# Performance work log

Hardware: AMD Instinct MI355X
Metric: run time of the kernel (lower is better)

Reference implementation:

```python
import jax, jax.numpy as jnp
import numpy as np

B, T, C, E = 2, 100, 80, 32
MH = MW = 64
IN_H = IN_W = 640.0
IOU_FACTOR, CLS_FACTOR, TOPK = 6.0, 0.5, 10
EPS = 1e-9


def get_anchors_and_scalers(fmaps, in_h, in_w):
    anchors, scalers = [], []
    for fh, fw in fmaps:
        stride = in_h / fh
        ys = (np.arange(fh) + 0.5) * stride
        xs = (np.arange(fw) + 0.5) * stride
        gy, gx = np.meshgrid(ys, xs, indexing='ij')
        anchors.append(np.stack([gx, gy], -1).reshape(-1, 2))
        scalers.append(np.full(fh * fw, stride))
    return (np.concatenate(anchors).astype(np.float32),
            np.concatenate(scalers).astype(np.float32))


def setup_inputs() -> dict:
    key = jax.random.key(0)
    ks = jax.random.split(key, 8)
    anchors_np, scalers_np = get_anchors_and_scalers([(80, 80), (40, 40), (20, 20)], IN_H, IN_W)
    anchors = jnp.asarray(anchors_np)
    scalers = jnp.asarray(scalers_np)
    A = anchors.shape[0]
    cls_logits = jax.random.normal(ks[0], (B, A, C), jnp.float32)
    wh = jax.random.uniform(ks[1], (B, A, 2), jnp.float32, 16.0, 160.0)
    ctr = anchors[None] + jax.random.normal(ks[2], (B, A, 2), jnp.float32) * 8.0
    pred_boxes = jnp.clip(jnp.concatenate([ctr - wh / 2, ctr + wh / 2], -1), 0.0, IN_W)
    mask_embs = jax.random.normal(ks[3], (B, A, E), jnp.float32)
    protos = jax.random.normal(ks[4], (B, MH, MW, E), jnp.float32)
    tl = jax.random.uniform(ks[5], (B, T, 2), jnp.float32, 0.0, 560.0)
    twh = jax.random.uniform(ks[6], (B, T, 2), jnp.float32, 30.0, 240.0)
    target_bbox = jnp.concatenate([tl, jnp.minimum(tl + twh, IN_W)], -1)
    target_cls = jax.random.randint(ks[7], (B, T), 0, C, jnp.int32)
    target_masks = (jax.random.uniform(jax.random.fold_in(key, 7), (B, MH, MW, T)) > 0.5).astype(jnp.float32)
    return {'cls_logits': cls_logits, 'pred_boxes': pred_boxes, 'mask_embs': mask_embs,
            'protos': protos, 'target_cls': target_cls, 'target_bbox': target_bbox,
            'target_masks': target_masks, 'anchors': anchors, 'scalers': scalers}


def _ciou_pairwise(gt, pr):
    # gt [B,T,4], pr [B,A,4] -> [B,T,A]
    g = gt[:, :, None, :]
    p = pr[:, None, :, :]
    ix1 = jnp.maximum(g[..., 0], p[..., 0]); iy1 = jnp.maximum(g[..., 1], p[..., 1])
    ix2 = jnp.minimum(g[..., 2], p[..., 2]); iy2 = jnp.minimum(g[..., 3], p[..., 3])
    inter = jnp.clip(ix2 - ix1, 0.0) * jnp.clip(iy2 - iy1, 0.0)
    wg = g[..., 2] - g[..., 0]; hg = g[..., 3] - g[..., 1]
    wp = p[..., 2] - p[..., 0]; hp = p[..., 3] - p[..., 1]
    union = wg * hg + wp * hp - inter + EPS
    iou = inter / union
    cw = jnp.maximum(g[..., 2], p[..., 2]) - jnp.minimum(g[..., 0], p[..., 0])
    ch = jnp.maximum(g[..., 3], p[..., 3]) - jnp.minimum(g[..., 1], p[..., 1])
    c2 = cw * cw + ch * ch + EPS
    rho2 = ((g[..., 0] + g[..., 2] - p[..., 0] - p[..., 2]) ** 2 +
            (g[..., 1] + g[..., 3] - p[..., 1] - p[..., 3]) ** 2) / 4.0
    v = (4.0 / (jnp.pi ** 2)) * (jnp.arctan(wg / (hg + EPS)) - jnp.arctan(wp / (hp + EPS))) ** 2
    alpha = jax.lax.stop_gradient(v / (1.0 - iou + v + EPS))
    return iou - rho2 / c2 - alpha * v


def _bbox_mask(boxes, mh, mw, in_h, in_w):
    # boxes [B,A,4] pixel xyxy -> [B,A,mh,mw] binary inside-box mask on mask grid
    sx, sy = mw / in_w, mh / in_h
    x1, y1, x2, y2 = boxes[..., 0] * sx, boxes[..., 1] * sy, boxes[..., 2] * sx, boxes[..., 3] * sy
    rows = jnp.arange(mh, dtype=boxes.dtype)
    cols = jnp.arange(mw, dtype=boxes.dtype)
    rm = (rows >= y1[..., None]) & (rows < y2[..., None])  # [B,A,mh]
    cm = (cols >= x1[..., None]) & (cols < x2[..., None])  # [B,A,mw]
    return (rm[..., :, None] & cm[..., None, :]).astype(boxes.dtype)


def _assign_and_build(cls_logits, pred_boxes, mask_embs, protos,
                      target_cls, target_bbox, target_masks, anchors, scalers):
    Bn, A, Cn = cls_logits.shape
    mh, mw = protos.shape[1], protos.shape[2]
    # --- task-aligned assigner ---
    lt, rb = target_bbox[:, :, None, :2], target_bbox[:, :, None, 2:]
    deltas = jnp.concatenate([anchors[None, None] - lt, rb - anchors[None, None]], -1)
    grid_mask = (jnp.min(deltas, -1) > 0).astype(cls_logits.dtype)  # [B,T,A]
    iou_mat = jnp.clip(_ciou_pairwise(target_bbox, pred_boxes), 0.0, 1.0)  # [B,T,A]
    cls_prob = jax.nn.sigmoid(cls_logits)  # [B,A,C]
    oh_t = jax.nn.one_hot(target_cls, Cn, dtype=cls_prob.dtype)  # [B,T,C]
    cls_mat = jnp.einsum('btc,bac->bta', oh_t, cls_prob)  # [B,T,A]
    tmat = grid_mask * (iou_mat ** IOU_FACTOR) * (cls_mat ** CLS_FACTOR)
    kth = jax.lax.top_k(tmat, TOPK)[0][..., -1:]  # [B,T,1]
    topk_targets = jnp.where((tmat >= kth) & (tmat > 0), tmat, 0.0)
    unique_idx = jnp.argmax(topk_targets, axis=1)  # [B,A] best GT per anchor
    valid = (jnp.sum(topk_targets, axis=1) > 0).astype(cls_logits.dtype)  # [B,A]
    align_bbox = jnp.take_along_axis(target_bbox, jnp.broadcast_to(unique_idx[..., None], (Bn, A, 4)), axis=1)
    align_cls_idx = jnp.take_along_axis(target_cls, unique_idx, axis=1)  # [B,A]
    max_target = jnp.max(tmat, axis=-1, keepdims=True)
    max_iou = jnp.max(iou_mat, axis=-1, keepdims=True)
    norm_term = tmat / (max_target + EPS) * max_iou  # [B,T,A]
    norm_g = jnp.take_along_axis(jnp.transpose(norm_term, (0, 2, 1)), unique_idx[..., None], axis=2)  # [B,A,1]
    align_cls = jax.nn.one_hot(align_cls_idx, Cn, dtype=cls_logits.dtype) * norm_g * valid[..., None]
    # --- loss-target assembly (compute_loss body) ---
    align_bbox_scaled = align_bbox / scalers[None, :, None]
    boxes_scaled = pred_boxes / scalers[None, :, None]
    box_target = jnp.concatenate([align_bbox_scaled, valid[..., None], align_cls], -1)
    box_mask = _bbox_mask(align_bbox, mh, mw, IN_H, IN_W)  # [B,A,mh,mw]
    valid_seg = box_mask * valid[..., None, None]
    seg_pred = jax.nn.sigmoid(jnp.einsum('bne,bhwe->bnhw', mask_embs, protos)) * valid_seg
    seg_pred = seg_pred.reshape(Bn, A, mh * mw)
    masks_t = jnp.transpose(target_masks, (0, 3, 1, 2))  # [B,T,mh,mw]
    idx4 = jnp.broadcast_to(unique_idx[..., None, None], (Bn, A, mh, mw))
    align_seg = (jnp.take_along_axis(masks_t, idx4, axis=1) * valid_seg).reshape(Bn, A, mh * mw)
    area = ((align_bbox[..., 2] - align_bbox[..., 0]) * (align_bbox[..., 3] - align_bbox[..., 1])
            / (IN_W * IN_H))
    seg_target = jnp.concatenate([area[..., None], valid[..., None], align_seg], -1)
    return jnp.concatenate([boxes_scaled, cls_logits, box_target, seg_pred, seg_target], -1)


def reference(cls_logits, pred_boxes, mask_embs, protos, target_cls, target_bbox,
              target_masks, anchors, scalers):
    return _assign_and_build(cls_logits, pred_boxes, mask_embs, protos,
                             target_cls, target_bbox, target_masks, anchors, scalers)
```

## Files before the change

kernel.cpp:

```cpp
#include <hip/hip_runtime.h>
#include <math.h>

#define A_TOT 8400
#define B_N   2
#define T_N   100
#define C_N   80
#define E_N   32
#define MH_N  64
#define MW_N  64
#define ROW_N 8363
#define NROWS (B_N*A_TOT)
#define EPSF  1e-9f
#define PARAM_STRIDE 12
#define COMP_CAP 1536
#define NEGINF -1e30f

__global__ __launch_bounds__(256) void k_prep(
    const float* __restrict__ pred_boxes, const float* __restrict__ target_bbox,
    float* __restrict__ pred_atan, float* __restrict__ tgt_atan) {
  int i = blockIdx.x * 256 + threadIdx.x;
  if (i < NROWS) {
    float4 pb = *(const float4*)(pred_boxes + (size_t)i*4);
    pred_atan[i] = atanf((pb.z - pb.x) / ((pb.w - pb.y) + EPSF));
  }
  if (i < B_N*T_N) {
    float4 g = *(const float4*)(target_bbox + i*4);
    tgt_atan[i] = atanf((g.z - g.x) / ((g.w - g.y) + EPSF));
  }
}

__device__ __forceinline__ float2 tmat_eval(
    float gx1, float gy1, float gx2, float gy2,
    float ax,  float ay,
    float px1, float py1, float px2, float py2,
    float cl, float atg, float atp) {
  float ix1 = fmaxf(gx1,px1), iy1 = fmaxf(gy1,py1);
  float ix2 = fminf(gx2,px2), iy2 = fminf(gy2,py2);
  float inter = fmaxf(ix2-ix1,0.f) * fmaxf(iy2-iy1,0.f);
  float wg = gx2-gx1, hg = gy2-gy1, wp = px2-px1, hp = py2-py1;
  float uni = wg*hg + wp*hp - inter + EPSF;
  float iou = inter / uni;
  float cw = fmaxf(gx2,px2) - fminf(gx1,px1);
  float ch = fmaxf(gy2,py2) - fminf(gy1,py1);
  float c2 = cw*cw + ch*ch + EPSF;
  float dx = gx1+gx2-px1-px2, dy = gy1+gy2-py1-py2;
  float rho2 = (dx*dx + dy*dy) * 0.25f;
  float da = atg - atp;
  float v  = 0.4052847345693511f * da * da;
  float alpha = v / (1.f - iou + v + EPSF);
  float ciou = iou - rho2/c2 - alpha*v;
  float iouc = fminf(fmaxf(ciou, 0.f), 1.f);

  float tm = 0.f;
  if (ax > gx1 && ay > gy1 && ax < gx2 && ay < gy2) {
    float cp = 1.f / (1.f + expf(-cl));
    float i2 = iouc * iouc;
    tm = i2*i2*i2 * sqrtf(cp);
  }
  return make_float2(tm, iouc);
}

__global__ __launch_bounds__(512) void k_score(
    const float* __restrict__ cls_logits, const float* __restrict__ pred_boxes,
    const float* __restrict__ target_bbox, const int* __restrict__ target_cls,
    const float* __restrict__ anchors,
    const float* __restrict__ pred_atan, const float* __restrict__ tgt_atan,
    float* __restrict__ tmat,
    float* __restrict__ kth, float* __restrict__ maxt, float* __restrict__ maxiou) {
  int bt   = blockIdx.x;
  int b    = bt / T_N;
  int tid  = threadIdx.x;
  int lane = tid & 63, wid = tid >> 6;
  __shared__ float comp[COMP_CAP];
  __shared__ float redm[8], redi[8];
  __shared__ float wtop[8][10];
  __shared__ int   cnt;
  if (tid == 0) cnt = 0;
  __syncthreads();

  float4 g  = *(const float4*)(target_bbox + bt*4);
  int    tc = target_cls[bt];
  float atg = tgt_atan[bt];
  float* trow = tmat + (size_t)bt * A_TOT;

  float lm = 0.f, li = 0.f;
  for (int a = tid; a < A_TOT; a += 512) {
    float ax = anchors[a*2+0], ay = anchors[a*2+1];
    float4 pb = *(const float4*)(pred_boxes + ((size_t)(b*A_TOT+a))*4);
    float cl = cls_logits[((size_t)(b*A_TOT+a))*C_N + tc];
    float2 r = tmat_eval(g.x,g.y,g.z,g.w, ax,ay, pb.x,pb.y,pb.z,pb.w,
                         cl, atg, pred_atan[b*A_TOT + a]);
    trow[a] = r.x;
    li = fmaxf(li, r.y);
    if (r.x > 0.f) {
      lm = fmaxf(lm, r.x);
      comp[atomicAdd(&cnt, 1)] = r.x;
    }
  }
  #pragma unroll
  for (int off = 32; off; off >>= 1) {
    lm = fmaxf(lm, __shfl_xor(lm, off));
    li = fmaxf(li, __shfl_xor(li, off));
  }
  if (lane == 0) { redm[wid] = lm; redi[wid] = li; }
  __syncthreads();
  if (tid == 0) {
    float m = redm[0], mi = redi[0];
    #pragma unroll
    for (int w = 1; w < 8; w++) { m = fmaxf(m, redm[w]); mi = fmaxf(mi, redi[w]); }
    maxt[bt] = m; maxiou[bt] = mi;
  }
  int count = cnt;

  int base = wid*64 + lane;
  float e0 = (base        < count) ? comp[base]        : NEGINF;
  float e1 = (base + 512  < count) ? comp[base + 512]  : NEGINF;
  float e2 = (base + 1024 < count) ? comp[base + 1024] : NEGINF;
  float mytop = NEGINF;
  #pragma unroll
  for (int k = 0; k < 10; k++) {
    float bv = e0; int bs = 0;
    if (e1 > bv) { bv = e1; bs = 1; }
    if (e2 > bv) { bv = e2; bs = 2; }
    float v = bv; int id = (lane << 2) | bs;
    #pragma unroll
    for (int off = 32; off; off >>= 1) {
      float ov = __shfl_xor(v, off); int oid = __shfl_xor(id, off);
      if (ov > v || (ov == v && oid < id)) { v = ov; id = oid; }
    }
    if ((id >> 2) == lane) {
      int s = id & 3;
      if (s == 0) e0 = NEGINF; else if (s == 1) e1 = NEGINF; else e2 = NEGINF;
    }
    if (lane == k) mytop = v;
  }
  if (lane < 10) wtop[wid][lane] = mytop;
  __syncthreads();

  if (wid == 0) {
    int ia = lane, ib = 64 + lane;
    float f0 = wtop[ia/10][ia%10];
    float f1 = (ib < 80) ? wtop[ib/10][ib%10] : NEGINF;
    float cur = NEGINF;
    #pragma unroll
    for (int k = 0; k < 10; k++) {
      float bv = f0; int bs = 0;
      if (f1 > bv) { bv = f1; bs = 1; }
      float v = bv; int id = (lane << 1) | bs;
      #pragma unroll
      for (int off = 32; off; off >>= 1) {
        float ov = __shfl_xor(v, off); int oid = __shfl_xor(id, off);
        if (ov > v || (ov == v && oid < id)) { v = ov; id = oid; }
      }
      if ((id >> 1) == lane) { if ((id & 1) == 0) f0 = NEGINF; else f1 = NEGINF; }
      cur = v;
    }
    if (lane == 0) kth[bt] = fmaxf(cur, 0.f);
  }
}

__global__ __launch_bounds__(64) void k_assign(
    const float* __restrict__ tmat,
    const float* __restrict__ kth, const float* __restrict__ maxt, const float* __restrict__ maxiou,
    const float* __restrict__ target_bbox, const int* __restrict__ target_cls,
    const float* __restrict__ scalers,
    float* __restrict__ params) {
  int b   = blockIdx.y;
  int tid = threadIdx.x;
  int a   = blockIdx.x * 64 + tid;
  __shared__ float kths[T_N];
  for (int i = tid; i < T_N; i += 64) kths[i] = kth[b*T_N + i];
  __syncthreads();
  if (a >= A_TOT) return;

  const float* col = tmat + (size_t)b * T_N * A_TOT + a;
  float best = 0.f; int u = 0, any = 0;
  #pragma unroll 4
  for (int t = 0; t < T_N; t++) {
    float v = col[(size_t)t * A_TOT];
    if (v > 0.f && v >= kths[t]) {
      any = 1;
      if (v > best) { best = v; u = t; }
    }
  }
  int bu = b*T_N + u;
  float ng = any ? best / (maxt[bu] + EPSF) * maxiou[bu] : 0.f;
  float4 tb = *(const float4*)(target_bbox + bu*4);
  float s = scalers[a];
  float area = (tb.z - tb.x) * (tb.w - tb.y) / (640.f*640.f);

  int row = b*A_TOT + a;
  float* pp = params + (size_t)row * PARAM_STRIDE;
  *(float4*)pp       = tb;
  *(float4*)(pp + 4) = make_float4(any ? 1.f : 0.f, ng, s, area);
  *(float4*)(pp + 8) = make_float4(__int_as_float(u), __int_as_float(target_cls[bu]), 0.f, 0.f);
}

__global__ __launch_bounds__(256) void k_sparse(
    const float* __restrict__ cls_logits, const float* __restrict__ pred_boxes,
    const float* __restrict__ mask_embs,  const float* __restrict__ protos,
    const float* __restrict__ t_masks,    const float* __restrict__ params,
    float* __restrict__ out) {
  unsigned row = blockIdx.x;
  int b   = row >= (unsigned)A_TOT;
  int tid = threadIdx.x;
  __shared__ float semb[E_N];

  const float* pp = params + (size_t)row * PARAM_STRIDE;
  float4 P0 = *(const float4*)pp;
  float4 P1 = *(const float4*)(pp + 4);
  int u  = __float_as_int(pp[8]);
  int ct = __float_as_int(pp[9]);
  bool valid = P1.x > 0.5f;
  size_t base = (size_t)row * ROW_N;

  if (tid < 92) {
    if (tid < 4) out[base + tid] = pred_boxes[(size_t)row*4 + tid] / P1.z;
    else if (tid < 84) out[base + tid] = cls_logits[(size_t)row*C_N + (tid-4)];
    else if (tid < 88) {
      float t = (tid==84)?P0.x:((tid==85)?P0.y:((tid==86)?P0.z:P0.w));
      out[base + tid] = t / P1.z;
    }
    else if (tid == 88) out[base + 88] = P1.x;
    else if (tid == 89) { if (valid) out[base + 89 + ct] = P1.y; }
    else if (tid == 90) out[base + 4265] = P1.w;
    else                out[base + 4266] = P1.x;
  }
  if (!valid) return;
  if (tid < E_N) semb[tid] = mask_embs[(size_t)row * E_N + tid];
  __syncthreads();

  float x1s = P0.x*0.1f, y1s = P0.y*0.1f, x2s = P0.z*0.1f, y2s = P0.w*0.1f;
  for (int p = tid; p < MH_N*MW_N; p += 256) {
    int h = p >> 6, w = p & 63;
    float fh = (float)h, fw = (float)w;
    if (fh >= y1s && fh < y2s && fw >= x1s && fw < x2s) {
      const float* pr = protos + ((size_t)((b*MH_N + h)*MW_N + w)) * E_N;
      float acc = 0.f;
      #pragma unroll
      for (int e = 0; e < E_N; e++) acc += semb[e] * pr[e];
      out[base + 169  + p] = 1.f / (1.f + expf(-acc));
      out[base + 4267 + p] = t_masks[((size_t)((b*MH_N + h)*MW_N + w)) * T_N + u];
    }
  }
}

extern "C" void kernel_launch(void* const* d_in, const int* in_sizes, int n_in,
                              void* d_out, int out_size, void* d_ws, size_t ws_size,
                              hipStream_t stream) {
  const float* cls_logits   = (const float*)d_in[0];
  const float* pred_boxes   = (const float*)d_in[1];
  const float* mask_embs    = (const float*)d_in[2];
  const float* protos       = (const float*)d_in[3];
  const int*   target_cls   = (const int*)  d_in[4];
  const float* target_bbox  = (const float*)d_in[5];
  const float* target_masks = (const float*)d_in[6];
  const float* anchors      = (const float*)d_in[7];
  const float* scalers      = (const float*)d_in[8];
  float* out = (float*)d_out;

  float* ws        = (float*)d_ws;
  float* kth       = ws;
  float* maxt      = kth    + B_N*T_N;
  float* maxiou    = maxt   + B_N*T_N;
  float* params    = ws + 600;
  float* tmat      = params + (size_t)NROWS*PARAM_STRIDE;
  float* pred_atan = tmat + (size_t)B_N*T_N*A_TOT;
  float* tgt_atan  = pred_atan + NROWS;

  hipMemsetAsync(out, 0, (size_t)NROWS * ROW_N * sizeof(float), stream);
  k_prep<<<(NROWS + 255)/256, 256, 0, stream>>>(pred_boxes, target_bbox,
                                                pred_atan, tgt_atan);
  k_score<<<B_N*T_N, 512, 0, stream>>>(cls_logits, pred_boxes, target_bbox,
                                       target_cls, anchors, pred_atan, tgt_atan,
                                       tmat, kth, maxt, maxiou);
  dim3 gAsn((A_TOT + 63)/64, B_N);
  k_assign<<<gAsn, 64, 0, stream>>>(tmat, kth, maxt, maxiou, target_bbox,
                                    target_cls, scalers, params);
  k_sparse<<<NROWS, 256, 0, stream>>>(cls_logits, pred_boxes, mask_embs, protos,
                                      target_masks, params, out);
}
```

Before: 190.5 us.

## Split scoring across anchor chunks, fuse assign into row writer, drop output memset

Scoring now runs per (target, anchor chunk) with per-chunk top-10 and max partials, and a small merge kernel combines them. That gives more parallel blocks than one block per target. The assign step is folded into the per-row output kernel, which now writes every element of its row, zeros included, using vectorized nontemporal stores. This removes the full-output memset and the params round trip. The cost is that each row block now does a 100-way column gather from tmat, and the top-10 loop uses serialized block reductions.

```diff
diff --git a/kernel.cpp b/kernel.cpp
--- a/kernel.cpp
+++ b/kernel.cpp
@@ -11,9 +11,12 @@
 #define ROW_N 8363
 #define NROWS (B_N*A_TOT)
 #define EPSF  1e-9f
-#define PARAM_STRIDE 12
-#define COMP_CAP 1536
+#define NCHUNK 4
+#define CHUNK_A 2100
+#define COMP_CAP 1280
 #define NEGINF -1e30f
+
+typedef float vfloat4 __attribute__((ext_vector_type(4)));
 
 __global__ __launch_bounds__(256) void k_prep(
     const float* __restrict__ pred_boxes, const float* __restrict__ target_bbox,
@@ -60,21 +63,20 @@
   return make_float2(tm, iouc);
 }
 
-__global__ __launch_bounds__(512) void k_score(
+__global__ __launch_bounds__(256) void k_score(
     const float* __restrict__ cls_logits, const float* __restrict__ pred_boxes,
     const float* __restrict__ target_bbox, const int* __restrict__ target_cls,
     const float* __restrict__ anchors,
     const float* __restrict__ pred_atan, const float* __restrict__ tgt_atan,
-    float* __restrict__ tmat,
-    float* __restrict__ kth, float* __restrict__ maxt, float* __restrict__ maxiou) {
-  int bt   = blockIdx.x;
-  int b    = bt / T_N;
-  int tid  = threadIdx.x;
-  int lane = tid & 63, wid = tid >> 6;
+    float* __restrict__ tmat, float* __restrict__ top10s,
+    float* __restrict__ pmaxt, float* __restrict__ pmaxi) {
+  int chunk = blockIdx.x;
+  int bt    = blockIdx.y;
+  int b     = bt / T_N;
+  int tid   = threadIdx.x;
   __shared__ float comp[COMP_CAP];
-  __shared__ float redm[8], redi[8];
-  __shared__ float wtop[8][10];
-  __shared__ int   cnt;
+  __shared__ float red[256];
+  __shared__ int   cnt, sidx;
   if (tid == 0) cnt = 0;
   __syncthreads();
 
@@ -83,8 +85,9 @@
   float atg = tgt_atan[bt];
   float* trow = tmat + (size_t)bt * A_TOT;
 
+  int a0 = chunk * CHUNK_A;
   float lm = 0.f, li = 0.f;
-  for (int a = tid; a < A_TOT; a += 512) {
+  for (int a = a0 + tid; a < a0 + CHUNK_A; a += 256) {
     float ax = anchors[a*2+0], ay = anchors[a*2+1];
     float4 pb = *(const float4*)(pred_boxes + ((size_t)(b*A_TOT+a))*4);
     float cl = cls_logits[((size_t)(b*A_TOT+a))*C_N + tc];
@@ -94,155 +97,177 @@
     li = fmaxf(li, r.y);
     if (r.x > 0.f) {
       lm = fmaxf(lm, r.x);
-      comp[atomicAdd(&cnt, 1)] = r.x;
-    }
-  }
-  #pragma unroll
-  for (int off = 32; off; off >>= 1) {
-    lm = fmaxf(lm, __shfl_xor(lm, off));
-    li = fmaxf(li, __shfl_xor(li, off));
-  }
-  if (lane == 0) { redm[wid] = lm; redi[wid] = li; }
-  __syncthreads();
-  if (tid == 0) {
-    float m = redm[0], mi = redi[0];
-    #pragma unroll
-    for (int w = 1; w < 8; w++) { m = fmaxf(m, redm[w]); mi = fmaxf(mi, redi[w]); }
-    maxt[bt] = m; maxiou[bt] = mi;
-  }
-  int count = cnt;
-
-  int base = wid*64 + lane;
-  float e0 = (base        < count) ? comp[base]        : NEGINF;
-  float e1 = (base + 512  < count) ? comp[base + 512]  : NEGINF;
-  float e2 = (base + 1024 < count) ? comp[base + 1024] : NEGINF;
-  float mytop = NEGINF;
+      int i = atomicAdd(&cnt, 1);
+      if (i < COMP_CAP) comp[i] = r.x;
+    }
+  }
+  red[tid] = lm; __syncthreads();
+  for (int s = 128; s > 0; s >>= 1) { if (tid < s) red[tid] = fmaxf(red[tid], red[tid+s]); __syncthreads(); }
+  if (tid == 0) pmaxt[bt*NCHUNK + chunk] = red[0];
+  __syncthreads();
+  red[tid] = li; __syncthreads();
+  for (int s = 128; s > 0; s >>= 1) { if (tid < s) red[tid] = fmaxf(red[tid], red[tid+s]); __syncthreads(); }
+  if (tid == 0) pmaxi[bt*NCHUNK + chunk] = red[0];
+  __syncthreads();
+  int count = min(cnt, COMP_CAP);
+
+  float* t10 = top10s + ((size_t)bt*NCHUNK + chunk) * 10;
+  for (int k = 0; k < 10; k++) {
+    float l = NEGINF;
+    for (int i = tid; i < count; i += 256) l = fmaxf(l, comp[i]);
+    red[tid] = l; __syncthreads();
+    for (int s = 128; s > 0; s >>= 1) { if (tid < s) red[tid] = fmaxf(red[tid], red[tid+s]); __syncthreads(); }
+    float m = red[0];
+    if (tid == 0) sidx = 0x7fffffff;
+    __syncthreads();
+    if (m > NEGINF) {
+      for (int i = tid; i < count; i += 256) if (comp[i] == m) atomicMin(&sidx, i);
+    }
+    __syncthreads();
+    if (tid == 0) {
+      if (sidx != 0x7fffffff) comp[sidx] = NEGINF;
+      t10[k] = m;
+    }
+    __syncthreads();
+  }
+}
+
+__global__ __launch_bounds__(64) void k_merge(
+    const float* __restrict__ top10s, const float* __restrict__ pmaxt,
+    const float* __restrict__ pmaxi,
+    float* __restrict__ kth, float* __restrict__ maxt, float* __restrict__ maxiou) {
+  int bt = blockIdx.x;
+  int lane = threadIdx.x;
+  float cand = (lane < NCHUNK*10) ? top10s[(size_t)bt*NCHUNK*10 + lane] : NEGINF;
+  float cur = NEGINF;
   #pragma unroll
   for (int k = 0; k < 10; k++) {
-    float bv = e0; int bs = 0;
-    if (e1 > bv) { bv = e1; bs = 1; }
-    if (e2 > bv) { bv = e2; bs = 2; }
-    float v = bv; int id = (lane << 2) | bs;
+    float v = cand; int id = lane;
     #pragma unroll
     for (int off = 32; off; off >>= 1) {
       float ov = __shfl_xor(v, off); int oid = __shfl_xor(id, off);
       if (ov > v || (ov == v && oid < id)) { v = ov; id = oid; }
     }
-    if ((id >> 2) == lane) {
-      int s = id & 3;
-      if (s == 0) e0 = NEGINF; else if (s == 1) e1 = NEGINF; else e2 = NEGINF;
-    }
-    if (lane == k) mytop = v;
-  }
-  if (lane < 10) wtop[wid][lane] = mytop;
-  __syncthreads();
-
-  if (wid == 0) {
-    int ia = lane, ib = 64 + lane;
-    float f0 = wtop[ia/10][ia%10];
-    float f1 = (ib < 80) ? wtop[ib/10][ib%10] : NEGINF;
-    float cur = NEGINF;
-    #pragma unroll
-    for (int k = 0; k < 10; k++) {
-      float bv = f0; int bs = 0;
-      if (f1 > bv) { bv = f1; bs = 1; }
-      float v = bv; int id = (lane << 1) | bs;
-      #pragma unroll
-      for (int off = 32; off; off >>= 1) {
-        float ov = __shfl_xor(v, off); int oid = __shfl_xor(id, off);
-        if (ov > v || (ov == v && oid < id)) { v = ov; id = oid; }
-      }
-      if ((id >> 1) == lane) { if ((id & 1) == 0) f0 = NEGINF; else f1 = NEGINF; }
-      cur = v;
-    }
-    if (lane == 0) kth[bt] = fmaxf(cur, 0.f);
-  }
-}
-
-__global__ __launch_bounds__(64) void k_assign(
-    const float* __restrict__ tmat,
-    const float* __restrict__ kth, const float* __restrict__ maxt, const float* __restrict__ maxiou,
-    const float* __restrict__ target_bbox, const int* __restrict__ target_cls,
-    const float* __restrict__ scalers,
-    float* __restrict__ params) {
-  int b   = blockIdx.y;
-  int tid = threadIdx.x;
-  int a   = blockIdx.x * 64 + tid;
-  __shared__ float kths[T_N];
-  for (int i = tid; i < T_N; i += 64) kths[i] = kth[b*T_N + i];
-  __syncthreads();
-  if (a >= A_TOT) return;
-
-  const float* col = tmat + (size_t)b * T_N * A_TOT + a;
-  float best = 0.f; int u = 0, any = 0;
-  #pragma unroll 4
-  for (int t = 0; t < T_N; t++) {
-    float v = col[(size_t)t * A_TOT];
-    if (v > 0.f && v >= kths[t]) {
-      any = 1;
-      if (v > best) { best = v; u = t; }
-    }
-  }
-  int bu = b*T_N + u;
-  float ng = any ? best / (maxt[bu] + EPSF) * maxiou[bu] : 0.f;
-  float4 tb = *(const float4*)(target_bbox + bu*4);
-  float s = scalers[a];
-  float area = (tb.z - tb.x) * (tb.w - tb.y) / (640.f*640.f);
-
-  int row = b*A_TOT + a;
-  float* pp = params + (size_t)row * PARAM_STRIDE;
-  *(float4*)pp       = tb;
-  *(float4*)(pp + 4) = make_float4(any ? 1.f : 0.f, ng, s, area);
-  *(float4*)(pp + 8) = make_float4(__int_as_float(u), __int_as_float(target_cls[bu]), 0.f, 0.f);
-}
-
-__global__ __launch_bounds__(256) void k_sparse(
+    if (id == lane) cand = NEGINF;
+    cur = v;
+  }
+  float pm = (lane < NCHUNK) ? pmaxt[bt*NCHUNK + lane] : 0.f;
+  float pi = (lane < NCHUNK) ? pmaxi[bt*NCHUNK + lane] : 0.f;
+  #pragma unroll
+  for (int off = 32; off; off >>= 1) {
+    pm = fmaxf(pm, __shfl_xor(pm, off));
+    pi = fmaxf(pi, __shfl_xor(pi, off));
+  }
+  if (lane == 0) {
+    kth[bt]    = fmaxf(cur, 0.f);
+    maxt[bt]   = pm;
+    maxiou[bt] = pi;
+  }
+}
+
+__global__ __launch_bounds__(256) void k_row(
     const float* __restrict__ cls_logits, const float* __restrict__ pred_boxes,
     const float* __restrict__ mask_embs,  const float* __restrict__ protos,
-    const float* __restrict__ t_masks,    const float* __restrict__ params,
+    const float* __restrict__ t_masks,    const float* __restrict__ tmat,
+    const float* __restrict__ kth, const float* __restrict__ maxt,
+    const float* __restrict__ maxiou, const float* __restrict__ target_bbox,
+    const int* __restrict__ target_cls, const float* __restrict__ scalers,
     float* __restrict__ out) {
   unsigned row = blockIdx.x;
   int b   = row >= (unsigned)A_TOT;
+  int a   = (int)row - b*A_TOT;
   int tid = threadIdx.x;
+  __shared__ float sv[128];
+  __shared__ int   st[128];
   __shared__ float semb[E_N];
-
-  const float* pp = params + (size_t)row * PARAM_STRIDE;
-  float4 P0 = *(const float4*)pp;
-  float4 P1 = *(const float4*)(pp + 4);
-  int u  = __float_as_int(pp[8]);
-  int ct = __float_as_int(pp[9]);
-  bool valid = P1.x > 0.5f;
+  __shared__ float ctx[10];
+
+  if (tid < 128) {
+    float v = 0.f; int tt = 0x7fff;
+    if (tid < T_N) {
+      int bt = b*T_N + tid;
+      float tv = tmat[(size_t)bt*A_TOT + a];
+      if (tv > 0.f && tv >= kth[bt]) { v = tv; tt = tid; }
+    }
+    sv[tid] = v; st[tid] = tt;
+  }
+  if (tid < E_N) semb[tid] = mask_embs[(size_t)row*E_N + tid];
+  __syncthreads();
+  if (tid < 64) {
+    float v1 = sv[tid];    int t1 = st[tid];
+    float v2 = sv[tid+64]; int t2 = st[tid+64];
+    if (v2 > v1 || (v2 == v1 && t2 < t1)) { v1 = v2; t1 = t2; }
+    #pragma unroll
+    for (int off = 32; off; off >>= 1) {
+      float ov = __shfl_xor(v1, off); int ot = __shfl_xor(t1, off);
+      if (ov > v1 || (ov == v1 && ot < t1)) { v1 = ov; t1 = ot; }
+    }
+    if (tid == 0) {
+      int anyv = v1 > 0.f;
+      int u = anyv ? t1 : 0;
+      int bu = b*T_N + u;
+      float4 tb = *(const float4*)(target_bbox + bu*4);
+      float ng = anyv ? v1 / (maxt[bu] + EPSF) * maxiou[bu] : 0.f;
+      ctx[0]=tb.x; ctx[1]=tb.y; ctx[2]=tb.z; ctx[3]=tb.w;
+      ctx[4]= anyv ? 1.f : 0.f; ctx[5]=ng; ctx[6]=scalers[a];
+      ctx[7]= (tb.z-tb.x)*(tb.w-tb.y)/(640.f*640.f);
+      ctx[8]=__int_as_float(u); ctx[9]=__int_as_float(target_cls[bu]);
+    }
+  }
+  __syncthreads();
+  float tb0=ctx[0], tb1=ctx[1], tb2=ctx[2], tb3=ctx[3];
+  float vld=ctx[4], ng=ctx[5], s=ctx[6], area=ctx[7];
+  int   u  =__float_as_int(ctx[8]), ct=__float_as_int(ctx[9]);
+  bool valid = vld > 0.5f;
+  float x1s=tb0*0.1f, y1s=tb1*0.1f, x2s=tb2*0.1f, y2s=tb3*0.1f;
   size_t base = (size_t)row * ROW_N;
 
-  if (tid < 92) {
-    if (tid < 4) out[base + tid] = pred_boxes[(size_t)row*4 + tid] / P1.z;
-    else if (tid < 84) out[base + tid] = cls_logits[(size_t)row*C_N + (tid-4)];
-    else if (tid < 88) {
-      float t = (tid==84)?P0.x:((tid==85)?P0.y:((tid==86)?P0.z:P0.w));
-      out[base + tid] = t / P1.z;
-    }
-    else if (tid == 88) out[base + 88] = P1.x;
-    else if (tid == 89) { if (valid) out[base + 89 + ct] = P1.y; }
-    else if (tid == 90) out[base + 4265] = P1.w;
-    else                out[base + 4266] = P1.x;
-  }
-  if (!valid) return;
-  if (tid < E_N) semb[tid] = mask_embs[(size_t)row * E_N + tid];
-  __syncthreads();
-
-  float x1s = P0.x*0.1f, y1s = P0.y*0.1f, x2s = P0.z*0.1f, y2s = P0.w*0.1f;
-  for (int p = tid; p < MH_N*MW_N; p += 256) {
-    int h = p >> 6, w = p & 63;
-    float fh = (float)h, fw = (float)w;
-    if (fh >= y1s && fh < y2s && fw >= x1s && fw < x2s) {
+  auto val = [&](unsigned p) -> float {
+    if (p < 84u) {
+      if (p < 4u) return pred_boxes[(size_t)row*4 + p] / s;
+      return cls_logits[(size_t)row*C_N + (p-4u)];
+    }
+    if (p < 169u) {
+      if (p < 88u) { float t=(p==84u)?tb0:((p==85u)?tb1:((p==86u)?tb2:tb3)); return t/s; }
+      if (p == 88u) return vld;
+      return (valid && (int)p - 89 == ct) ? ng : 0.f;
+    }
+    if (p < 4265u) {
+      if (!valid) return 0.f;
+      unsigned q = p - 169u; int h = q >> 6, w = q & 63;
+      float fh = (float)h, fw = (float)w;
+      if (!(fh >= y1s && fh < y2s && fw >= x1s && fw < x2s)) return 0.f;
       const float* pr = protos + ((size_t)((b*MH_N + h)*MW_N + w)) * E_N;
       float acc = 0.f;
       #pragma unroll
       for (int e = 0; e < E_N; e++) acc += semb[e] * pr[e];
-      out[base + 169  + p] = 1.f / (1.f + expf(-acc));
-      out[base + 4267 + p] = t_masks[((size_t)((b*MH_N + h)*MW_N + w)) * T_N + u];
-    }
-  }
+      return 1.f / (1.f + expf(-acc));
+    }
+    if (p == 4265u) return area;
+    if (p == 4266u) return vld;
+    if (!valid) return 0.f;
+    unsigned q = p - 4267u; int h = q >> 6, w = q & 63;
+    float fh = (float)h, fw = (float)w;
+    if (!(fh >= y1s && fh < y2s && fw >= x1s && fw < x2s)) return 0.f;
+    return t_masks[((size_t)((b*MH_N + h)*MW_N + w)) * T_N + u];
+  };
+
+  unsigned head = (4u - ((row * (unsigned)ROW_N) & 3u)) & 3u;
+  if (tid < (int)head) out[base + tid] = val(tid);
+  unsigned vec_end = head + (((unsigned)ROW_N - head) & ~3u);
+  for (unsigned p = head + 4u*(unsigned)tid; p < vec_end; p += 1024u) {
+    vfloat4 o;
+    bool pure = (p >= 4267u) || (p >= 169u && p + 4u <= 4265u);
+    if (pure && !valid) {
+      o = (vfloat4)(0.f);
+    } else {
+      o.x = val(p); o.y = val(p+1u); o.z = val(p+2u); o.w = val(p+3u);
+    }
+    __builtin_nontemporal_store(o, (vfloat4*)(out + base + p));
+  }
+  unsigned tail_n = (unsigned)ROW_N - vec_end;
+  if (tid >= 32 && tid < 32 + (int)tail_n)
+    out[base + vec_end + (unsigned)(tid - 32)] = val(vec_end + (unsigned)(tid - 32));
 }
 
 extern "C" void kernel_launch(void* const* d_in, const int* in_sizes, int n_in,
@@ -260,23 +285,24 @@
   float* out = (float*)d_out;
 
   float* ws        = (float*)d_ws;
-  float* kth       = ws;
-  float* maxt      = kth    + B_N*T_N;
-  float* maxiou    = maxt   + B_N*T_N;
-  float* params    = ws + 600;
-  float* tmat      = params + (size_t)NROWS*PARAM_STRIDE;
+  float* tmat      = ws;
   float* pred_atan = tmat + (size_t)B_N*T_N*A_TOT;
   float* tgt_atan  = pred_atan + NROWS;
-
-  hipMemsetAsync(out, 0, (size_t)NROWS * ROW_N * sizeof(float), stream);
+  float* top10s    = tgt_atan + B_N*T_N;
+  float* pmaxt     = top10s + (size_t)B_N*T_N*NCHUNK*10;
+  float* pmaxi     = pmaxt + B_N*T_N*NCHUNK;
+  float* kth       = pmaxi + B_N*T_N*NCHUNK;
+  float* maxt      = kth + B_N*T_N;
+  float* maxiou    = maxt + B_N*T_N;
+
   k_prep<<<(NROWS + 255)/256, 256, 0, stream>>>(pred_boxes, target_bbox,
                                                 pred_atan, tgt_atan);
-  k_score<<<B_N*T_N, 512, 0, stream>>>(cls_logits, pred_boxes, target_bbox,
-                                       target_cls, anchors, pred_atan, tgt_atan,
-                                       tmat, kth, maxt, maxiou);
-  dim3 gAsn((A_TOT + 63)/64, B_N);
-  k_assign<<<gAsn, 64, 0, stream>>>(tmat, kth, maxt, maxiou, target_bbox,
-                                    target_cls, scalers, params);
-  k_sparse<<<NROWS, 256, 0, stream>>>(cls_logits, pred_boxes, mask_embs, protos,
-                                      target_masks, params, out);
-}
+  dim3 gS(NCHUNK, B_N*T_N);
+  k_score<<<gS, 256, 0, stream>>>(cls_logits, pred_boxes, target_bbox,
+                                  target_cls, anchors, pred_atan, tgt_atan,
+                                  tmat, top10s, pmaxt, pmaxi);
+  k_merge<<<B_N*T_N, 64, 0, stream>>>(top10s, pmaxt, pmaxi, kth, maxt, maxiou);
+  k_row<<<NROWS, 256, 0, stream>>>(cls_logits, pred_boxes, mask_embs, protos,
+                                   target_masks, tmat, kth, maxt, maxiou,
+                                   target_bbox, target_cls, scalers, out);
+}
```

Measured after the change: 189.5 us. Within noise of the previous version (-0.5%).
